# Performance work log

Measured on AMD Instinct MI355X. Metric: run time of the kernel, lower is better.

## Reference

```python
import jax, jax.numpy as jnp
import numpy as np
from jax import lax

B, C, H, W = 4, 192, 64, 64
D_STATE, D_CONV, EXPAND = 16, 4, 2
D_INNER = EXPAND * C           # 384
DT_RANK = (C + 15) // 16       # 12 (mamba_ssm default ceil(d_model/16))


def setup_inputs() -> dict:
    key = jax.random.key(0)
    ks = jax.random.split(key, 12)
    sc = lambda k, shape, s=0.02: (jax.random.normal(k, shape, jnp.float32) * s)
    x = jax.random.normal(ks[0], (B, C, H, W), jnp.float32)
    norm_w = jnp.ones((C,), jnp.float32)
    norm_b = jnp.zeros((C,), jnp.float32)
    in_proj_w = sc(ks[1], (2 * D_INNER, C))
    conv_w = sc(ks[2], (D_INNER, D_CONV), 0.1)
    conv_b = jnp.zeros((D_INNER,), jnp.float32)
    x_proj_w = sc(ks[3], (DT_RANK + 2 * D_STATE, D_INNER))
    dt_proj_w = sc(ks[4], (D_INNER, DT_RANK), 0.1)
    # dt bias init so softplus(dt_bias) is in a realistic [1e-3, 1e-1] range
    dt0 = jax.random.uniform(ks[5], (D_INNER,), jnp.float32, 0.001, 0.1)
    dt_proj_b = jnp.log(jnp.expm1(dt0))
    A_log = jnp.log(jnp.broadcast_to(
        jnp.arange(1, D_STATE + 1, dtype=jnp.float32), (D_INNER, D_STATE)))
    D = jnp.ones((D_INNER,), jnp.float32)
    out_proj_w = sc(ks[6], (C, D_INNER))
    return {"x": x, "norm_w": norm_w, "norm_b": norm_b, "in_proj_w": in_proj_w,
            "conv_w": conv_w, "conv_b": conv_b, "x_proj_w": x_proj_w,
            "dt_proj_w": dt_proj_w, "dt_proj_b": dt_proj_b, "A_log": A_log,
            "D": D, "out_proj_w": out_proj_w}


def _mamba2d(x, norm_w, norm_b, in_proj_w, conv_w, conv_b, x_proj_w,
             dt_proj_w, dt_proj_b, A_log, D, out_proj_w):
    b, c, h, w = x.shape
    L = h * w
    seq = x.reshape(b, c, L).transpose(0, 2, 1)            # (B, L, C)
    # LayerNorm over channel dim
    mu = seq.mean(-1, keepdims=True)
    var = ((seq - mu) ** 2).mean(-1, keepdims=True)
    seqn = (seq - mu) * lax.rsqrt(var + 1e-5) * norm_w + norm_b
    # in_proj -> (x, z)
    xz = seqn @ in_proj_w.T                                # (B, L, 2*d_inner)
    xin, z = jnp.split(xz, 2, axis=-1)
    # causal depthwise conv1d over L
    xc = xin.transpose(0, 2, 1)                            # (B, d_inner, L)
    xc = lax.conv_general_dilated(xc, conv_w[:, None, :], (1,),
                                  [(D_CONV - 1, 0)],
                                  feature_group_count=D_INNER)
    xc = jax.nn.silu(xc + conv_b[None, :, None])
    xs = xc.transpose(0, 2, 1)                             # (B, L, d_inner)
    # input-dependent dt, B, C
    dbl = xs @ x_proj_w.T                                  # (B, L, dt_rank+2n)
    dt = dbl[..., :DT_RANK]
    Bm = dbl[..., DT_RANK:DT_RANK + D_STATE]               # (B, L, n)
    Cm = dbl[..., DT_RANK + D_STATE:]                      # (B, L, n)
    dt = jax.nn.softplus(dt @ dt_proj_w.T + dt_proj_b)     # (B, L, d_inner)
    A = -jnp.exp(A_log)                                    # (d_inner, n)
    dA = jnp.exp(dt[..., None] * A)                        # (B, L, d_inner, n)
    dBx = jnp.einsum('bld,bln->bldn', dt * xs, Bm)         # (B, L, d_inner, n)
    # selective scan over L
    def step(hcar, inp):
        dA_t, dBx_t, C_t = inp
        hcar = dA_t * hcar + dBx_t                         # (B, d_inner, n)
        y_t = jnp.einsum('bdn,bn->bd', hcar, C_t)
        return hcar, y_t
    h0 = jnp.zeros((b, D_INNER, D_STATE), xs.dtype)
    _, ys = lax.scan(step, h0, (jnp.moveaxis(dA, 1, 0),
                                jnp.moveaxis(dBx, 1, 0),
                                jnp.moveaxis(Cm, 1, 0)))
    y = jnp.moveaxis(ys, 0, 1) + xs * D                    # (B, L, d_inner)
    y = y * jax.nn.silu(z)
    out = y @ out_proj_w.T                                 # (B, L, C)
    return x + out.transpose(0, 2, 1).reshape(b, c, h, w)


def reference(x, norm_w, norm_b, in_proj_w, conv_w, conv_b, x_proj_w,
              dt_proj_w, dt_proj_b, A_log, D, out_proj_w):
    return _mamba2d(x, norm_w, norm_b, in_proj_w, conv_w, conv_b, x_proj_w,
                    dt_proj_w, dt_proj_b, A_log, D, out_proj_w)
```

## Files before the change

kernel.cpp:

```cpp
#include <hip/hip_runtime.h>
#include <hip/hip_bf16.h>

constexpr int B_ = 4;
constexpr int C_ = 192;
constexpr int L_ = 4096;
constexpr int DI = 384;
constexpr int DSs = 16;
constexpr int DTR = 12;
constexpr int NDBL = 44;
constexpr int NCHUNK = 128;
constexpr int CSZ = 32;
constexpr int NSUP = 8;

constexpr size_t BL = (size_t)B_ * L_;

constexpr size_t F_SEQN = 0;
constexpr size_t F_XIN  = F_SEQN + BL * C_ / 2;
constexpr size_t F_Z    = F_XIN + BL * DI / 2;
constexpr size_t F_XSB  = F_Z + BL * DI / 2;
constexpr size_t F_DBL  = F_XSB + BL * DI / 2;
constexpr size_t F_DT   = F_DBL + BL * NDBL;
constexpr size_t F_SBUF = F_DT + BL * DI / 2;
constexpr size_t F_HLOC = F_SBUF + (size_t)B_ * NCHUNK * DI;
constexpr size_t F_SPRE = F_HLOC + (size_t)B_ * NCHUNK * DI * 16 / 2;
constexpr size_t F_HSUP = F_SPRE + (size_t)B_ * NCHUNK * DI;
constexpr size_t F_SSUP = F_HSUP + (size_t)B_ * NSUP * 16 * DI;
constexpr size_t F_ISUP = F_SSUP + (size_t)B_ * NSUP * DI;
constexpr size_t F_WBUF = F_ISUP + (size_t)B_ * NSUP * 16 * DI;

typedef __attribute__((ext_vector_type(8))) short bf16x8;
typedef __attribute__((ext_vector_type(4))) float f32x4;

__device__ __forceinline__ unsigned short f2bf(float v) {
  unsigned x = __builtin_bit_cast(unsigned, v);
  unsigned r = x + 0x7FFFu + ((x >> 16) & 1u);
  return (unsigned short)(r >> 16);
}
__device__ __forceinline__ float bf2f(unsigned short u) {
  return __builtin_bit_cast(float, (unsigned)u << 16);
}
__device__ __forceinline__ void gload16(const void* g, void* l) {
  __builtin_amdgcn_global_load_lds((const __attribute__((address_space(1))) void*)g,
                                   (__attribute__((address_space(3))) void*)l, 16, 0, 0);
}
#define MFMA16(a, b, c) __builtin_amdgcn_mfma_f32_16x16x32_bf16(a, b, c, 0, 0, 0)

__global__ __launch_bounds__(256) void k_ln(const float* __restrict__ x,
                                            const float* __restrict__ nw,
                                            const float* __restrict__ nb,
                                            unsigned short* __restrict__ seqn,
                                            const float* __restrict__ ipw,
                                            const float* __restrict__ xpw,
                                            const float* __restrict__ opw,
                                            unsigned short* __restrict__ wbuf) {
  if (blockIdx.x >= 1024) {
    int t = (blockIdx.x - 1024) * 256 + threadIdx.x;
    if (t < 239616) {
      float v;
      if (t < 147456) v = ipw[t];
      else if (t < 165888) {
        int j = t - 147456;
        int r = j / 384, c = j - r * 384;
        v = (r < 44) ? xpw[r * 384 + c] : 0.f;
      } else v = opw[t - 165888];
      wbuf[t] = f2bf(v);
    }
    return;
  }
  __shared__ unsigned short xt[192][18];
  __shared__ float ps[16][16], ps2[16][16];
  __shared__ float mu_[16], rs_[16];
  __shared__ float wsh[192], bsh[192];
  int tid = threadIdx.x;
  int blk = blockIdx.x;
  int b = blk >> 8;
  int l0 = (blk & 255) << 4;
  const float* xb = x + (size_t)b * C_ * L_;
  for (int idx = tid; idx < 192 * 4; idx += 256) {
    int c = idx >> 2, lq = idx & 3;
    float4 v = *(const float4*)&xb[(size_t)c * L_ + l0 + (lq << 2)];
    ushort2 u0, u1;
    u0.x = f2bf(v.x); u0.y = f2bf(v.y);
    u1.x = f2bf(v.z); u1.y = f2bf(v.w);
    *(ushort2*)&xt[c][(lq << 2)] = u0;
    *(ushort2*)&xt[c][(lq << 2) + 2] = u1;
  }
  if (tid < 192) { wsh[tid] = nw[tid]; bsh[tid] = nb[tid]; }
  __syncthreads();
  int ll = tid & 15, q = tid >> 4;
  float s = 0.f, ss = 0.f;
  for (int c = q * 12; c < q * 12 + 12; ++c) {
    float v = bf2f(xt[c][ll]);
    s += v; ss += v * v;
  }
  ps[q][ll] = s; ps2[q][ll] = ss;
  __syncthreads();
  if (q == 0) {
    float st = 0.f, sst = 0.f;
#pragma unroll
    for (int g = 0; g < 16; ++g) { st += ps[g][ll]; sst += ps2[g][ll]; }
    float mu = st * (1.f / 192.f);
    float var = sst * (1.f / 192.f) - mu * mu;
    mu_[ll] = mu; rs_[ll] = rsqrtf(var + 1e-5f);
  }
  __syncthreads();
  unsigned short* so = seqn + ((size_t)b * L_ + l0) * C_;
  for (int idx = tid; idx < 16 * 192; idx += 256) {
    int l = idx / 192, c = idx - l * 192;
    so[idx] = f2bf((bf2f(xt[c][l]) - mu_[l]) * rs_[l] * wsh[c] + bsh[c]);
  }
}

__global__ __launch_bounds__(256) void k_inproj(const unsigned short* __restrict__ A,
                                                const unsigned short* __restrict__ W,
                                                unsigned short* __restrict__ xin,
                                                unsigned short* __restrict__ z) {
  __shared__ unsigned short smem[16384];
  unsigned short* As = smem;
  unsigned short* Bs = smem + 8192;
  int tid = threadIdx.x;
  int w = tid >> 6, l = tid & 63;
  int wr = w >> 1, wc = w & 1;
  int m0 = blockIdx.x << 7;
  int n0 = blockIdx.y << 7;
  f32x4 acc[4][4];
#pragma unroll
  for (int i = 0; i < 4; ++i)
#pragma unroll
    for (int j = 0; j < 4; ++j) acc[i][j] = (f32x4){0.f, 0.f, 0.f, 0.f};
  int lr = l & 15, lk = l >> 4;
  for (int kt = 0; kt < 3; ++kt) {
    int k0 = kt * 64;
    if (kt) __syncthreads();
#pragma unroll
    for (int i = 0; i < 4; ++i) {
      int row = (i << 5) + (tid >> 3);
      int gc = k0 + (((tid & 7) ^ (row & 7)) << 3);
      gload16(A + (size_t)(m0 + row) * 192 + gc, &As[(i << 11) + (w << 9)]);
      gload16(W + (size_t)(n0 + row) * 192 + gc, &Bs[(i << 11) + (w << 9)]);
    }
    __syncthreads();
#pragma unroll
    for (int ks = 0; ks < 2; ++ks) {
      int s = (ks << 2) + lk;
      bf16x8 af[4], bfr[4];
#pragma unroll
      for (int mi = 0; mi < 4; ++mi) {
        int r = (wr << 6) + (mi << 4) + lr;
        af[mi] = *(const bf16x8*)&As[r * 64 + ((s ^ (r & 7)) << 3)];
      }
#pragma unroll
      for (int ni = 0; ni < 4; ++ni) {
        int r = (wc << 6) + (ni << 4) + lr;
        bfr[ni] = *(const bf16x8*)&Bs[r * 64 + ((s ^ (r & 7)) << 3)];
      }
#pragma unroll
      for (int mi = 0; mi < 4; ++mi)
#pragma unroll
        for (int ni = 0; ni < 4; ++ni) acc[mi][ni] = MFMA16(af[mi], bfr[ni], acc[mi][ni]);
    }
  }
  __syncthreads();
#pragma unroll
  for (int mi = 0; mi < 4; ++mi)
#pragma unroll
    for (int ni = 0; ni < 4; ++ni) {
      int col = (wc << 6) + (ni << 4) + lr;
#pragma unroll
      for (int r = 0; r < 4; ++r) {
        int row = (wr << 6) + (mi << 4) + (lk << 2) + r;
        smem[(row << 7) + col] = f2bf(acc[mi][ni][r]);
      }
    }
  __syncthreads();
#pragma unroll
  for (int i = 0; i < 8; ++i) {
    int chunk = i * 256 + tid;
    int row = chunk >> 4, cq = chunk & 15;
    int n = n0 + (cq << 3);
    unsigned short* dst = (n < 384) ? (xin + (size_t)(m0 + row) * DI + n)
                                    : (z + (size_t)(m0 + row) * DI + (n - 384));
    *(bf16x8*)dst = *(const bf16x8*)&smem[(row << 7) + (cq << 3)];
  }
}

__global__ __launch_bounds__(384) void k_convx(const unsigned short* __restrict__ xin,
                                               const float* __restrict__ cw,
                                               const float* __restrict__ cb,
                                               const unsigned short* __restrict__ W,
                                               const float* __restrict__ dw,
                                               const float* __restrict__ dbias,
                                               const float* __restrict__ A_log,
                                               unsigned short* __restrict__ xsb,
                                               float* __restrict__ dbl,
                                               unsigned short* __restrict__ dtb,
                                               unsigned short* __restrict__ Hloc,
                                               float* __restrict__ Sbuf) {
  __shared__ unsigned short xs[6 * 2048];
  __shared__ unsigned short Bs[3072];
  __shared__ float dl[CSZ][12];
  __shared__ float Bsh2[CSZ][16];
  int tid = threadIdx.x;
  int w = tid >> 6, l = tid & 63;
  int b = blockIdx.y;
  int chunk = blockIdx.x;
  int l0 = chunk << 5;
  int d = tid;
  float4 w4 = *(const float4*)&cw[d * 4];
  float bb = cb[d];
  const unsigned short* xp = xin + ((size_t)b * L_ + l0) * DI + d;
  unsigned short* op = xsb + ((size_t)b * L_ + l0) * DI + d;
  float x0 = 0.f, x1 = 0.f, x2 = 0.f;
  if (l0 > 0) {
    x0 = bf2f(*(xp - 3 * DI));
    x1 = bf2f(*(xp - 2 * DI));
    x2 = bf2f(*(xp - DI));
  }
  int kt = d >> 6, col = d & 63, g = col >> 3, e = col & 7;
  unsigned short* xsrow = xs + kt * 2048;
  for (int r = 0; r < 32; ++r) {
    float xv = bf2f(xp[(size_t)r * DI]);
    float a = bb + w4.x * x0 + w4.y * x1 + w4.z * x2 + w4.w * xv;
    float sv = a * __builtin_amdgcn_rcpf(1.f + __expf(-a));
    unsigned short sb = f2bf(sv);
    xsrow[r * 64 + ((g ^ (r & 7)) << 3) + e] = sb;
    op[(size_t)r * DI] = sb;
    x0 = x1; x1 = x2; x2 = xv;
  }
  __syncthreads();
  int lr = l & 15, lk = l >> 4;
  f32x4 acc[3];
#pragma unroll
  for (int i = 0; i < 3; ++i) acc[i] = (f32x4){0.f, 0.f, 0.f, 0.f};
  for (int kt2 = 0; kt2 < 6; ++kt2) {
    int k0 = kt2 * 64;
    if (kt2) __syncthreads();
    {
      int row = tid >> 3;
      int gc = k0 + (((tid & 7) ^ (row & 7)) << 3);
      gload16(W + (size_t)row * 384 + gc, &Bs[w << 9]);
    }
    __syncthreads();
    if (w < 2) {
#pragma unroll
      for (int ks = 0; ks < 2; ++ks) {
        int s = (ks << 2) + lk;
        int ar = (w << 4) + lr;
        bf16x8 a = *(const bf16x8*)&xs[kt2 * 2048 + ar * 64 + ((s ^ (ar & 7)) << 3)];
#pragma unroll
        for (int ni = 0; ni < 3; ++ni) {
          int br = (ni << 4) + lr;
          bf16x8 bbv = *(const bf16x8*)&Bs[br * 64 + ((s ^ (br & 7)) << 3)];
          acc[ni] = MFMA16(a, bbv, acc[ni]);
        }
      }
    }
  }
  if (w < 2) {
#pragma unroll
    for (int ni = 0; ni < 3; ++ni)
#pragma unroll
      for (int r = 0; r < 4; ++r) {
        int colq = (ni << 4) + lr;
        int row = (w << 4) + (lk << 2) + r;
        float v = acc[ni][r];
        if (colq < NDBL) dbl[((size_t)b * L_ + l0 + row) * NDBL + colq] = v;
        if (colq < 12) dl[row][colq] = v;
        else if (colq < 28) Bsh2[row][colq - 12] = v;
      }
  }
  __syncthreads();
  float4 wv0 = *(const float4*)&dw[d * 12];
  float4 wv1 = *(const float4*)&dw[d * 12 + 4];
  float4 wv2 = *(const float4*)&dw[d * 12 + 8];
  float bias = dbias[d];
  bool fast = true;
#pragma unroll
  for (int n = 0; n < 16; ++n) {
    float An_ = -__expf(A_log[d * 16 + n]);
    fast = fast && (fabsf(An_ + (float)(n + 1)) < 2e-3f);
  }
  unsigned short* dtp = dtb + ((size_t)b * L_ + l0) * DI + d;
  float h[16];
#pragma unroll
  for (int n = 0; n < 16; ++n) h[n] = 0.f;
  float S = 0.f;
  if (fast) {
#pragma unroll
    for (int i = 0; i < CSZ; ++i) {
      float4 c0 = *(const float4*)&dl[i][0];
      float4 c1 = *(const float4*)&dl[i][4];
      float4 c2 = *(const float4*)&dl[i][8];
      float a = bias;
      a = fmaf(wv0.x, c0.x, a); a = fmaf(wv0.y, c0.y, a);
      a = fmaf(wv0.z, c0.z, a); a = fmaf(wv0.w, c0.w, a);
      a = fmaf(wv1.x, c1.x, a); a = fmaf(wv1.y, c1.y, a);
      a = fmaf(wv1.z, c1.z, a); a = fmaf(wv1.w, c1.w, a);
      a = fmaf(wv2.x, c2.x, a); a = fmaf(wv2.y, c2.y, a);
      a = fmaf(wv2.z, c2.z, a); a = fmaf(wv2.w, c2.w, a);
      float sp = fmaxf(a, 0.f) + __logf(1.f + __expf(-fabsf(a)));
      dtp[(size_t)i * DI] = f2bf(sp);
      S += sp;
      float xv = bf2f(xsrow[i * 64 + ((g ^ (i & 7)) << 3) + e]);
      float dtx = sp * xv;
      float r = __expf(-sp);
      float r2 = r * r;
      float r4 = r2 * r2;
      float dA0 = r, dA1 = r2, dA2 = r2 * r, dA3 = r4;
#pragma unroll
      for (int gg = 0; gg < 4; ++gg) {
        float4 Bg = *(const float4*)&Bsh2[i][gg << 2];
        h[(gg << 2) + 0] = fmaf(dA0, h[(gg << 2) + 0], dtx * Bg.x);
        h[(gg << 2) + 1] = fmaf(dA1, h[(gg << 2) + 1], dtx * Bg.y);
        h[(gg << 2) + 2] = fmaf(dA2, h[(gg << 2) + 2], dtx * Bg.z);
        h[(gg << 2) + 3] = fmaf(dA3, h[(gg << 2) + 3], dtx * Bg.w);
        if (gg < 3) { dA0 *= r4; dA1 *= r4; dA2 *= r4; dA3 *= r4; }
      }
    }
  } else {
    float An[16];
#pragma unroll
    for (int n = 0; n < 16; ++n) An[n] = -__expf(A_log[d * 16 + n]);
#pragma unroll
    for (int i = 0; i < CSZ; ++i) {
      float4 c0 = *(const float4*)&dl[i][0];
      float4 c1 = *(const float4*)&dl[i][4];
      float4 c2 = *(const float4*)&dl[i][8];
      float a = bias;
      a = fmaf(wv0.x, c0.x, a); a = fmaf(wv0.y, c0.y, a);
      a = fmaf(wv0.z, c0.z, a); a = fmaf(wv0.w, c0.w, a);
      a = fmaf(wv1.x, c1.x, a); a = fmaf(wv1.y, c1.y, a);
      a = fmaf(wv1.z, c1.z, a); a = fmaf(wv1.w, c1.w, a);
      a = fmaf(wv2.x, c2.x, a); a = fmaf(wv2.y, c2.y, a);
      a = fmaf(wv2.z, c2.z, a); a = fmaf(wv2.w, c2.w, a);
      float sp = fmaxf(a, 0.f) + __logf(1.f + __expf(-fabsf(a)));
      dtp[(size_t)i * DI] = f2bf(sp);
      S += sp;
      float xv = bf2f(xsrow[i * 64 + ((g ^ (i & 7)) << 3) + e]);
      float dtx = sp * xv;
#pragma unroll
      for (int n = 0; n < 16; ++n)
        h[n] = fmaf(__expf(sp * An[n]), h[n], dtx * Bsh2[i][n]);
    }
  }
  size_t hbase = ((size_t)(b * NCHUNK + chunk) * 16) * DI + d;
#pragma unroll
  for (int n = 0; n < 16; ++n) Hloc[hbase + (size_t)n * DI] = f2bf(h[n]);
  Sbuf[((size_t)b * NCHUNK + chunk) * DI + d] = S;
}

__global__ __launch_bounds__(384) void k_scanB1(const float* __restrict__ A_log,
                                                unsigned short* __restrict__ Hloc,
                                                const float* __restrict__ Sbuf,
                                                float* __restrict__ Spre,
                                                float* __restrict__ Hsup,
                                                float* __restrict__ Ssup) {
  int d = threadIdx.x;
  int blk = blockIdx.x;
  int n = blk & 15;
  int s = (blk >> 4) & 7;
  int b = blk >> 7;
  float An = -__expf(A_log[d * 16 + n]);
  float h = 0.f, Sp = 0.f;
  int c0 = s * 16;
#pragma unroll
  for (int i = 0; i < 16; ++i) {
    int c = c0 + i;
    size_t hidx = (((size_t)(b * NCHUNK + c) * 16) + n) * DI + d;
    float Hl = bf2f(Hloc[hidx]);
    float S = Sbuf[((size_t)b * NCHUNK + c) * DI + d];
    Hloc[hidx] = f2bf(h);
    if (n == 0) Spre[((size_t)b * NCHUNK + c) * DI + d] = Sp;
    h = fmaf(__expf(An * S), h, Hl);
    Sp += S;
  }
  Hsup[(((size_t)(b * NSUP + s) * 16) + n) * DI + d] = h;
  if (n == 0) Ssup[((size_t)b * NSUP + s) * DI + d] = Sp;
}

__global__ __launch_bounds__(384) void k_scanB2(const float* __restrict__ A_log,
                                                const float* __restrict__ Hsup,
                                                const float* __restrict__ Ssup,
                                                float* __restrict__ Isup) {
  int d = threadIdx.x;
  int blk = blockIdx.x;
  int n = blk & 15;
  int b = blk >> 4;
  float An = -__expf(A_log[d * 16 + n]);
  float I = 0.f;
#pragma unroll
  for (int s = 0; s < NSUP; ++s) {
    size_t idx = (((size_t)(b * NSUP + s) * 16) + n) * DI + d;
    Isup[idx] = I;
    I = fmaf(__expf(An * Ssup[((size_t)b * NSUP + s) * DI + d]), I, Hsup[idx]);
  }
}

__global__ __launch_bounds__(384) void k_scanC(const unsigned short* __restrict__ xsb,
                                               const unsigned short* __restrict__ dtb,
                                               const float* __restrict__ dbl,
                                               const unsigned short* __restrict__ z,
                                               const float* __restrict__ A_log,
                                               const float* __restrict__ Dw,
                                               const unsigned short* __restrict__ Hloc,
                                               const float* __restrict__ Spre,
                                               const float* __restrict__ Isup,
                                               const unsigned short* __restrict__ Wo,
                                               const float* __restrict__ x,
                                               float* __restrict__ out) {
  __shared__ float BCsh[CSZ][32];
  __shared__ unsigned short yt[6 * 2048];
  __shared__ unsigned short Bs[12288];
  int tid = threadIdx.x;
  int blk = blockIdx.x;
  int b = blk >> 7;
  int chunk = blk & (NCHUNK - 1);
  int l0 = chunk << 5;
  for (int idx = tid; idx < CSZ * 32; idx += 384) {
    int r = idx >> 5, n32 = idx & 31;
    BCsh[r][n32] = dbl[((size_t)b * L_ + l0 + r) * NDBL + DTR + n32];
  }
  int d = tid;
  float Dd = Dw[d];
  bool fast = true;
#pragma unroll
  for (int n = 0; n < 16; ++n) {
    float An_ = -__expf(A_log[d * 16 + n]);
    fast = fast && (fabsf(An_ + (float)(n + 1)) < 2e-3f);
  }
  int sup = chunk >> 4;
  size_t hbase = ((size_t)(b * NCHUNK + chunk) * 16) * DI + d;
  size_t ibase = ((size_t)(b * NSUP + sup) * 16) * DI + d;
  float Spv = Spre[((size_t)b * NCHUNK + chunk) * DI + d];
  float h[16];
  if (fast) {
    float t = __expf(-Spv);
    float t2 = t * t;
    float t4 = t2 * t2;
    float p0 = t, p1 = t2, p2 = t2 * t, p3 = t4;
#pragma unroll
    for (int g = 0; g < 4; ++g) {
      h[(g << 2) + 0] = fmaf(p0, Isup[ibase + (size_t)((g << 2) + 0) * DI],
                             bf2f(Hloc[hbase + (size_t)((g << 2) + 0) * DI]));
      h[(g << 2) + 1] = fmaf(p1, Isup[ibase + (size_t)((g << 2) + 1) * DI],
                             bf2f(Hloc[hbase + (size_t)((g << 2) + 1) * DI]));
      h[(g << 2) + 2] = fmaf(p2, Isup[ibase + (size_t)((g << 2) + 2) * DI],
                             bf2f(Hloc[hbase + (size_t)((g << 2) + 2) * DI]));
      h[(g << 2) + 3] = fmaf(p3, Isup[ibase + (size_t)((g << 2) + 3) * DI],
                             bf2f(Hloc[hbase + (size_t)((g << 2) + 3) * DI]));
      if (g < 3) { p0 *= t4; p1 *= t4; p2 *= t4; p3 *= t4; }
    }
  } else {
#pragma unroll
    for (int n = 0; n < 16; ++n) {
      float An_ = -__expf(A_log[d * 16 + n]);
      h[n] = fmaf(__expf(An_ * Spv), Isup[ibase + (size_t)n * DI],
                  bf2f(Hloc[hbase + (size_t)n * DI]));
    }
  }
  const unsigned short* xp = xsb + ((size_t)b * L_ + l0) * DI + d;
  const unsigned short* dtp = dtb + ((size_t)b * L_ + l0) * DI + d;
  const unsigned short* zp = z + ((size_t)b * L_ + l0) * DI + d;
  int ktile = d >> 6, colq = d & 63, gq = colq >> 3, eq = colq & 7;
  unsigned short* ytp = yt + ktile * 2048;
  __syncthreads();
  if (fast) {
#pragma unroll
    for (int i = 0; i < CSZ; ++i) {
      float sp = bf2f(dtp[(size_t)i * DI]);
      float xv = bf2f(xp[(size_t)i * DI]);
      float zv = bf2f(zp[(size_t)i * DI]);
      float dtx = sp * xv;
      float r = __expf(-sp);
      float r2 = r * r;
      float r4 = r2 * r2;
      float dA0 = r, dA1 = r2, dA2 = r2 * r, dA3 = r4;
      float y = 0.f;
#pragma unroll
      for (int g = 0; g < 4; ++g) {
        float4 Bg = *(const float4*)&BCsh[i][g << 2];
        float4 Cg = *(const float4*)&BCsh[i][16 + (g << 2)];
        h[(g << 2) + 0] = fmaf(dA0, h[(g << 2) + 0], dtx * Bg.x);
        h[(g << 2) + 1] = fmaf(dA1, h[(g << 2) + 1], dtx * Bg.y);
        h[(g << 2) + 2] = fmaf(dA2, h[(g << 2) + 2], dtx * Bg.z);
        h[(g << 2) + 3] = fmaf(dA3, h[(g << 2) + 3], dtx * Bg.w);
        y = fmaf(h[(g << 2) + 0], Cg.x, y);
        y = fmaf(h[(g << 2) + 1], Cg.y, y);
        y = fmaf(h[(g << 2) + 2], Cg.z, y);
        y = fmaf(h[(g << 2) + 3], Cg.w, y);
        if (g < 3) { dA0 *= r4; dA1 *= r4; dA2 *= r4; dA3 *= r4; }
      }
      y = fmaf(xv, Dd, y);
      float sig = __builtin_amdgcn_rcpf(1.f + __expf(-zv));
      ytp[i * 64 + ((gq ^ (i & 7)) << 3) + eq] = f2bf(y * (zv * sig));
    }
  } else {
    float An[16];
#pragma unroll
    for (int n = 0; n < 16; ++n) An[n] = -__expf(A_log[d * 16 + n]);
#pragma unroll
    for (int i = 0; i < CSZ; ++i) {
      float sp = bf2f(dtp[(size_t)i * DI]);
      float xv = bf2f(xp[(size_t)i * DI]);
      float zv = bf2f(zp[(size_t)i * DI]);
      float dtx = sp * xv;
      float y = 0.f;
#pragma unroll
      for (int n = 0; n < 16; ++n) {
        h[n] = fmaf(__expf(sp * An[n]), h[n], dtx * BCsh[i][n]);
        y = fmaf(h[n], BCsh[i][16 + n], y);
      }
      y = fmaf(xv, Dd, y);
      float sig = __builtin_amdgcn_rcpf(1.f + __expf(-zv));
      ytp[i * 64 + ((gq ^ (i & 7)) << 3) + eq] = f2bf(y * (zv * sig));
    }
  }
  int w = tid >> 6, l = tid & 63;
  int lr = l & 15, lk = l >> 4;
  int mt = w & 1;
  int ng = w >> 1;
  f32x4 acc[4];
#pragma unroll
  for (int j = 0; j < 4; ++j) acc[j] = (f32x4){0.f, 0.f, 0.f, 0.f};
  for (int kt = 0; kt < 6; ++kt) {
    int k0 = kt * 64;
    __syncthreads();
#pragma unroll
    for (int j = 0; j < 4; ++j) {
      int row = j * 48 + (tid >> 3);
      int gc = k0 + (((tid & 7) ^ (row & 7)) << 3);
      gload16(Wo + (size_t)row * 384 + gc, &Bs[j * 3072 + (w << 9)]);
    }
    __syncthreads();
#pragma unroll
    for (int ks = 0; ks < 2; ++ks) {
      int s = (ks << 2) + lk;
      bf16x8 a = *(const bf16x8*)&yt[kt * 2048 + (mt * 16 + lr) * 64 + ((s ^ (lr & 7)) << 3)];
#pragma unroll
      for (int j = 0; j < 4; ++j) {
        int br = (ng * 4 + j) * 16 + lr;
        bf16x8 bv = *(const bf16x8*)&Bs[br * 64 + ((s ^ (br & 7)) << 3)];
        acc[j] = MFMA16(a, bv, acc[j]);
      }
    }
  }
#pragma unroll
  for (int j = 0; j < 4; ++j) {
    int c = (ng * 4 + j) * 16 + lr;
    size_t off = ((size_t)b * C_ + c) * L_ + l0 + mt * 16 + (lk << 2);
    f32x4 xv = *(const f32x4*)&x[off];
    *(f32x4*)&out[off] = acc[j] + xv;
  }
}

extern "C" void kernel_launch(void* const* d_in, const int* in_sizes, int n_in,
                              void* d_out, int out_size, void* d_ws, size_t ws_size,
                              hipStream_t stream) {
  const float* x         = (const float*)d_in[0];
  const float* norm_w    = (const float*)d_in[1];
  const float* norm_b    = (const float*)d_in[2];
  const float* in_proj_w = (const float*)d_in[3];
  const float* conv_w    = (const float*)d_in[4];
  const float* conv_b    = (const float*)d_in[5];
  const float* x_proj_w  = (const float*)d_in[6];
  const float* dt_proj_w = (const float*)d_in[7];
  const float* dt_proj_b = (const float*)d_in[8];
  const float* A_log     = (const float*)d_in[9];
  const float* Dw        = (const float*)d_in[10];
  const float* out_proj_w= (const float*)d_in[11];
  float* out = (float*)d_out;
  float* ws = (float*)d_ws;

  unsigned short* seqn = (unsigned short*)(ws + F_SEQN);
  unsigned short* xin  = (unsigned short*)(ws + F_XIN);
  unsigned short* z    = (unsigned short*)(ws + F_Z);
  unsigned short* xsb  = (unsigned short*)(ws + F_XSB);
  float* dbl           = ws + F_DBL;
  unsigned short* dtb  = (unsigned short*)(ws + F_DT);
  float* Sbuf          = ws + F_SBUF;
  unsigned short* Hloc = (unsigned short*)(ws + F_HLOC);
  float* Spre          = ws + F_SPRE;
  float* Hsup          = ws + F_HSUP;
  float* Ssup          = ws + F_SSUP;
  float* Isup          = ws + F_ISUP;
  unsigned short* wbuf = (unsigned short*)(ws + F_WBUF);
  unsigned short* ipw  = wbuf;
  unsigned short* xpw  = wbuf + 147456;
  unsigned short* opw  = wbuf + 165888;

  hipLaunchKernelGGL(k_ln, dim3(1960), dim3(256), 0, stream, x, norm_w, norm_b, seqn,
                     in_proj_w, x_proj_w, out_proj_w, wbuf);
  hipLaunchKernelGGL(k_inproj, dim3(128, 6), dim3(256), 0, stream, seqn, ipw, xin, z);
  hipLaunchKernelGGL(k_convx, dim3(128, 4), dim3(384), 0, stream, xin, conv_w, conv_b, xpw,
                     dt_proj_w, dt_proj_b, A_log, xsb, dbl, dtb, Hloc, Sbuf);
  hipLaunchKernelGGL(k_scanB1, dim3(512), dim3(384), 0, stream, A_log, Hloc, Sbuf, Spre, Hsup,
                     Ssup);
  hipLaunchKernelGGL(k_scanB2, dim3(64), dim3(384), 0, stream, A_log, Hsup, Ssup, Isup);
  hipLaunchKernelGGL(k_scanC, dim3(512), dim3(384), 0, stream, xsb, dtb, dbl, z, A_log, Dw,
                     Hloc, Spre, Isup, opw, x, out);
}
```

Baseline: 97.23 us.

## Fold superchunk prefix scan into scanC and double-buffer weight tiles

Removes the k_scanB2 launch and has each k_scanC block recompute its superchunk prefix state by looping over earlier superchunk summaries in registers. The change targets one kernel launch and the Isup round-trip through global memory, at the cost of some redundant work in later chunks. The x_proj GEMM in k_convx and the out_proj GEMM in k_scanC now double-buffer their LDS weight tiles, so the next tile is prefetched while MFMAs run and one barrier per iteration goes away. The x_proj GEMM also spreads its work over all six waves with one accumulator each, where before only two waves did the MFMAs.

```diff
diff --git a/kernel.cpp b/kernel.cpp
--- a/kernel.cpp
+++ b/kernel.cpp
@@ -197,7 +197,7 @@
                                                unsigned short* __restrict__ Hloc,
                                                float* __restrict__ Sbuf) {
   __shared__ unsigned short xs[6 * 2048];
-  __shared__ unsigned short Bs[3072];
+  __shared__ unsigned short Bs[2][3072];
   __shared__ float dl[CSZ][12];
   __shared__ float Bsh2[CSZ][16];
   int tid = threadIdx.x;
@@ -229,45 +229,42 @@
   }
   __syncthreads();
   int lr = l & 15, lk = l >> 4;
-  f32x4 acc[3];
-#pragma unroll
-  for (int i = 0; i < 3; ++i) acc[i] = (f32x4){0.f, 0.f, 0.f, 0.f};
+  int mt = w & 1, nt = w >> 1;
+  {
+    int row = tid >> 3;
+    int gc = (((tid & 7) ^ (row & 7)) << 3);
+    gload16(W + (size_t)row * 384 + gc, &Bs[0][w << 9]);
+  }
+  f32x4 accx = (f32x4){0.f, 0.f, 0.f, 0.f};
   for (int kt2 = 0; kt2 < 6; ++kt2) {
-    int k0 = kt2 * 64;
-    if (kt2) __syncthreads();
-    {
+    __syncthreads();
+    if (kt2 < 5) {
+      int k0 = (kt2 + 1) * 64;
       int row = tid >> 3;
       int gc = k0 + (((tid & 7) ^ (row & 7)) << 3);
-      gload16(W + (size_t)row * 384 + gc, &Bs[w << 9]);
-    }
-    __syncthreads();
-    if (w < 2) {
-#pragma unroll
-      for (int ks = 0; ks < 2; ++ks) {
-        int s = (ks << 2) + lk;
-        int ar = (w << 4) + lr;
-        bf16x8 a = *(const bf16x8*)&xs[kt2 * 2048 + ar * 64 + ((s ^ (ar & 7)) << 3)];
-#pragma unroll
-        for (int ni = 0; ni < 3; ++ni) {
-          int br = (ni << 4) + lr;
-          bf16x8 bbv = *(const bf16x8*)&Bs[br * 64 + ((s ^ (br & 7)) << 3)];
-          acc[ni] = MFMA16(a, bbv, acc[ni]);
-        }
-      }
-    }
-  }
-  if (w < 2) {
-#pragma unroll
-    for (int ni = 0; ni < 3; ++ni)
-#pragma unroll
-      for (int r = 0; r < 4; ++r) {
-        int colq = (ni << 4) + lr;
-        int row = (w << 4) + (lk << 2) + r;
-        float v = acc[ni][r];
-        if (colq < NDBL) dbl[((size_t)b * L_ + l0 + row) * NDBL + colq] = v;
-        if (colq < 12) dl[row][colq] = v;
-        else if (colq < 28) Bsh2[row][colq - 12] = v;
-      }
+      gload16(W + (size_t)row * 384 + gc, &Bs[(kt2 + 1) & 1][w << 9]);
+    }
+    const unsigned short* Bcur = Bs[kt2 & 1];
+#pragma unroll
+    for (int ks = 0; ks < 2; ++ks) {
+      int s = (ks << 2) + lk;
+      int ar = (mt << 4) + lr;
+      bf16x8 a = *(const bf16x8*)&xs[kt2 * 2048 + ar * 64 + ((s ^ (ar & 7)) << 3)];
+      int br = (nt << 4) + lr;
+      bf16x8 bbv = *(const bf16x8*)&Bcur[br * 64 + ((s ^ (br & 7)) << 3)];
+      accx = MFMA16(a, bbv, accx);
+    }
+  }
+  {
+    int colq = (nt << 4) + lr;
+#pragma unroll
+    for (int r = 0; r < 4; ++r) {
+      int row = (mt << 4) + (lk << 2) + r;
+      float v = accx[r];
+      if (colq < NDBL) dbl[((size_t)b * L_ + l0 + row) * NDBL + colq] = v;
+      if (colq < 12) dl[row][colq] = v;
+      else if (colq < 28) Bsh2[row][colq - 12] = v;
+    }
   }
   __syncthreads();
   float4 wv0 = *(const float4*)&dw[d * 12];
@@ -378,24 +375,6 @@
   if (n == 0) Ssup[((size_t)b * NSUP + s) * DI + d] = Sp;
 }
 
-__global__ __launch_bounds__(384) void k_scanB2(const float* __restrict__ A_log,
-                                                const float* __restrict__ Hsup,
-                                                const float* __restrict__ Ssup,
-                                                float* __restrict__ Isup) {
-  int d = threadIdx.x;
-  int blk = blockIdx.x;
-  int n = blk & 15;
-  int b = blk >> 4;
-  float An = -__expf(A_log[d * 16 + n]);
-  float I = 0.f;
-#pragma unroll
-  for (int s = 0; s < NSUP; ++s) {
-    size_t idx = (((size_t)(b * NSUP + s) * 16) + n) * DI + d;
-    Isup[idx] = I;
-    I = fmaf(__expf(An * Ssup[((size_t)b * NSUP + s) * DI + d]), I, Hsup[idx]);
-  }
-}
-
 __global__ __launch_bounds__(384) void k_scanC(const unsigned short* __restrict__ xsb,
                                                const unsigned short* __restrict__ dtb,
                                                const float* __restrict__ dbl,
@@ -404,13 +383,14 @@
                                                const float* __restrict__ Dw,
                                                const unsigned short* __restrict__ Hloc,
                                                const float* __restrict__ Spre,
-                                               const float* __restrict__ Isup,
+                                               const float* __restrict__ Hsup,
+                                               const float* __restrict__ Ssup,
                                                const unsigned short* __restrict__ Wo,
                                                const float* __restrict__ x,
                                                float* __restrict__ out) {
   __shared__ float BCsh[CSZ][32];
   __shared__ unsigned short yt[6 * 2048];
-  __shared__ unsigned short Bs[12288];
+  __shared__ unsigned short Bs[2][12288];
   int tid = threadIdx.x;
   int blk = blockIdx.x;
   int b = blk >> 7;
@@ -430,33 +410,55 @@
   }
   int sup = chunk >> 4;
   size_t hbase = ((size_t)(b * NCHUNK + chunk) * 16) * DI + d;
-  size_t ibase = ((size_t)(b * NSUP + sup) * 16) * DI + d;
   float Spv = Spre[((size_t)b * NCHUNK + chunk) * DI + d];
   float h[16];
   if (fast) {
+    float I[16];
+#pragma unroll
+    for (int n = 0; n < 16; ++n) I[n] = 0.f;
+    for (int s = 0; s < sup; ++s) {
+      float Ss = Ssup[((size_t)b * NSUP + s) * DI + d];
+      const float* Hs = Hsup + ((size_t)(b * NSUP + s) * 16) * DI + d;
+      float t = __expf(-Ss);
+      float t2 = t * t, t4 = t2 * t2;
+      float p0 = t, p1 = t2, p2 = t2 * t, p3 = t4;
+#pragma unroll
+      for (int gI = 0; gI < 4; ++gI) {
+        I[(gI << 2) + 0] = fmaf(p0, I[(gI << 2) + 0], Hs[(size_t)((gI << 2) + 0) * DI]);
+        I[(gI << 2) + 1] = fmaf(p1, I[(gI << 2) + 1], Hs[(size_t)((gI << 2) + 1) * DI]);
+        I[(gI << 2) + 2] = fmaf(p2, I[(gI << 2) + 2], Hs[(size_t)((gI << 2) + 2) * DI]);
+        I[(gI << 2) + 3] = fmaf(p3, I[(gI << 2) + 3], Hs[(size_t)((gI << 2) + 3) * DI]);
+        if (gI < 3) { p0 *= t4; p1 *= t4; p2 *= t4; p3 *= t4; }
+      }
+    }
     float t = __expf(-Spv);
-    float t2 = t * t;
-    float t4 = t2 * t2;
+    float t2 = t * t, t4 = t2 * t2;
     float p0 = t, p1 = t2, p2 = t2 * t, p3 = t4;
 #pragma unroll
-    for (int g = 0; g < 4; ++g) {
-      h[(g << 2) + 0] = fmaf(p0, Isup[ibase + (size_t)((g << 2) + 0) * DI],
-                             bf2f(Hloc[hbase + (size_t)((g << 2) + 0) * DI]));
-      h[(g << 2) + 1] = fmaf(p1, Isup[ibase + (size_t)((g << 2) + 1) * DI],
-                             bf2f(Hloc[hbase + (size_t)((g << 2) + 1) * DI]));
-      h[(g << 2) + 2] = fmaf(p2, Isup[ibase + (size_t)((g << 2) + 2) * DI],
-                             bf2f(Hloc[hbase + (size_t)((g << 2) + 2) * DI]));
-      h[(g << 2) + 3] = fmaf(p3, Isup[ibase + (size_t)((g << 2) + 3) * DI],
-                             bf2f(Hloc[hbase + (size_t)((g << 2) + 3) * DI]));
-      if (g < 3) { p0 *= t4; p1 *= t4; p2 *= t4; p3 *= t4; }
+    for (int gI = 0; gI < 4; ++gI) {
+      h[(gI << 2) + 0] = fmaf(p0, I[(gI << 2) + 0], bf2f(Hloc[hbase + (size_t)((gI << 2) + 0) * DI]));
+      h[(gI << 2) + 1] = fmaf(p1, I[(gI << 2) + 1], bf2f(Hloc[hbase + (size_t)((gI << 2) + 1) * DI]));
+      h[(gI << 2) + 2] = fmaf(p2, I[(gI << 2) + 2], bf2f(Hloc[hbase + (size_t)((gI << 2) + 2) * DI]));
+      h[(gI << 2) + 3] = fmaf(p3, I[(gI << 2) + 3], bf2f(Hloc[hbase + (size_t)((gI << 2) + 3) * DI]));
+      if (gI < 3) { p0 *= t4; p1 *= t4; p2 *= t4; p3 *= t4; }
     }
   } else {
-#pragma unroll
-    for (int n = 0; n < 16; ++n) {
-      float An_ = -__expf(A_log[d * 16 + n]);
-      h[n] = fmaf(__expf(An_ * Spv), Isup[ibase + (size_t)n * DI],
-                  bf2f(Hloc[hbase + (size_t)n * DI]));
-    }
+    float An[16];
+#pragma unroll
+    for (int n = 0; n < 16; ++n) An[n] = -__expf(A_log[d * 16 + n]);
+    float I[16];
+#pragma unroll
+    for (int n = 0; n < 16; ++n) I[n] = 0.f;
+    for (int s = 0; s < sup; ++s) {
+      float Ss = Ssup[((size_t)b * NSUP + s) * DI + d];
+      const float* Hs = Hsup + ((size_t)(b * NSUP + s) * 16) * DI + d;
+#pragma unroll
+      for (int n = 0; n < 16; ++n)
+        I[n] = fmaf(__expf(An[n] * Ss), I[n], Hs[(size_t)n * DI]);
+    }
+#pragma unroll
+    for (int n = 0; n < 16; ++n)
+      h[n] = fmaf(__expf(An[n] * Spv), I[n], bf2f(Hloc[hbase + (size_t)n * DI]));
   }
   const unsigned short* xp = xsb + ((size_t)b * L_ + l0) * DI + d;
   const unsigned short* dtp = dtb + ((size_t)b * L_ + l0) * DI + d;
@@ -519,19 +521,29 @@
   int lr = l & 15, lk = l >> 4;
   int mt = w & 1;
   int ng = w >> 1;
+  {
+#pragma unroll
+    for (int j = 0; j < 4; ++j) {
+      int row = j * 48 + (tid >> 3);
+      int gc = (((tid & 7) ^ (row & 7)) << 3);
+      gload16(Wo + (size_t)row * 384 + gc, &Bs[0][j * 3072 + (w << 9)]);
+    }
+  }
   f32x4 acc[4];
 #pragma unroll
   for (int j = 0; j < 4; ++j) acc[j] = (f32x4){0.f, 0.f, 0.f, 0.f};
   for (int kt = 0; kt < 6; ++kt) {
-    int k0 = kt * 64;
     __syncthreads();
-#pragma unroll
-    for (int j = 0; j < 4; ++j) {
-      int row = j * 48 + (tid >> 3);
-      int gc = k0 + (((tid & 7) ^ (row & 7)) << 3);
-      gload16(Wo + (size_t)row * 384 + gc, &Bs[j * 3072 + (w << 9)]);
-    }
-    __syncthreads();
+    if (kt < 5) {
+      int k0 = (kt + 1) * 64;
+#pragma unroll
+      for (int j = 0; j < 4; ++j) {
+        int row = j * 48 + (tid >> 3);
+        int gc = k0 + (((tid & 7) ^ (row & 7)) << 3);
+        gload16(Wo + (size_t)row * 384 + gc, &Bs[(kt + 1) & 1][j * 3072 + (w << 9)]);
+      }
+    }
+    const unsigned short* Bcur = Bs[kt & 1];
 #pragma unroll
     for (int ks = 0; ks < 2; ++ks) {
       int s = (ks << 2) + lk;
@@ -539,7 +551,7 @@
 #pragma unroll
       for (int j = 0; j < 4; ++j) {
         int br = (ng * 4 + j) * 16 + lr;
-        bf16x8 bv = *(const bf16x8*)&Bs[br * 64 + ((s ^ (br & 7)) << 3)];
+        bf16x8 bv = *(const bf16x8*)&Bcur[br * 64 + ((s ^ (br & 7)) << 3)];
         acc[j] = MFMA16(a, bv, acc[j]);
       }
     }
@@ -582,7 +594,6 @@
   float* Spre          = ws + F_SPRE;
   float* Hsup          = ws + F_HSUP;
   float* Ssup          = ws + F_SSUP;
-  float* Isup          = ws + F_ISUP;
   unsigned short* wbuf = (unsigned short*)(ws + F_WBUF);
   unsigned short* ipw  = wbuf;
   unsigned short* xpw  = wbuf + 147456;
@@ -595,7 +606,6 @@
                      dt_proj_w, dt_proj_b, A_log, xsb, dbl, dtb, Hloc, Sbuf);
   hipLaunchKernelGGL(k_scanB1, dim3(512), dim3(384), 0, stream, A_log, Hloc, Sbuf, Spre, Hsup,
                      Ssup);
-  hipLaunchKernelGGL(k_scanB2, dim3(64), dim3(384), 0, stream, A_log, Hsup, Ssup, Isup);
   hipLaunchKernelGGL(k_scanC, dim3(512), dim3(384), 0, stream, xsb, dtb, dbl, z, A_log, Dw,
-                     Hloc, Spre, Isup, opw, x, out);
-}
+                     Hloc, Spre, Hsup, Ssup, opw, x, out);
+}
```

After: 103.9 us. 6.9% more time.
